# Kernel optimization log

Hardware: AMD Instinct MI355X
Metric: run time of the kernel (lower is better)

Reference implementation:

```python
import jax, jax.numpy as jnp
import numpy as np

E, H, NH = 512, 2048, 8
HD = E // NH
EPS = 1e-5


def setup_inputs() -> dict:
    key = jax.random.key(0)
    ks = jax.random.split(key, 13)
    s = lambda k, shape, fan_in: jax.random.normal(k, shape, dtype=jnp.float32) * (1.0 / np.sqrt(fan_in))
    return {
        "x": jax.random.normal(ks[0], (1, 4096, E), dtype=jnp.float32),
        "ln_g": jnp.ones((E,), jnp.float32),
        "ln_b": jnp.zeros((E,), jnp.float32),
        "qkv_w": s(ks[1], (3 * E, E), E),
        "qkv_b": jnp.zeros((3 * E,), jnp.float32),
        "proj_w": s(ks[2], (E, E), E),
        "proj_b": jnp.zeros((E,), jnp.float32),
        "fc1_w": s(ks[3], (H, E), E),
        "fc1_b": jnp.zeros((H,), jnp.float32),
        "fc2_w": s(ks[4], (H, H), H),
        "fc2_b": jnp.zeros((H,), jnp.float32),
        "fc3_w": s(ks[5], (E, H), H),
        "fc3_b": jnp.zeros((E,), jnp.float32),
    }


def _layernorm(x, g, b):
    mu = jnp.mean(x, axis=-1, keepdims=True)
    var = jnp.mean(jnp.square(x - mu), axis=-1, keepdims=True)
    return (x - mu) * jax.lax.rsqrt(var + EPS) * g + b


def _attention(h, qkv_w, qkv_b, proj_w, proj_b):
    B, N, _ = h.shape
    qkv = h @ qkv_w.T + qkv_b                      # [B, N, 3E]
    qkv = qkv.reshape(B, N, 3, NH, HD).transpose(2, 0, 3, 1, 4)  # [3, B, NH, N, HD]
    q, k, v = qkv[0], qkv[1], qkv[2]
    scale = HD ** -0.5
    scores = jnp.einsum("bhqd,bhkd->bhqk", q, k) * scale  # full N x N matrix (faithful)
    probs = jax.nn.softmax(scores, axis=-1)
    out = jnp.einsum("bhqk,bhkd->bhqd", probs, v)  # [B, NH, N, HD]
    out = out.transpose(0, 2, 1, 3).reshape(B, N, E)
    return out @ proj_w.T + proj_b


def _mlp(h, fc1_w, fc1_b, fc2_w, fc2_b, fc3_w, fc3_b):
    h = jax.nn.relu(h @ fc1_w.T + fc1_b)
    h = jax.nn.relu(h @ fc2_w.T + fc2_b)
    return h @ fc3_w.T + fc3_b


def reference(x, ln_g, ln_b, qkv_w, qkv_b, proj_w, proj_b,
              fc1_w, fc1_b, fc2_w, fc2_b, fc3_w, fc3_b):
    # Pre-norm block; note the SAME LayerNorm params are used for both sublayers
    x = x + _attention(_layernorm(x, ln_g, ln_b), qkv_w, qkv_b, proj_w, proj_b)
    x = x + _mlp(_layernorm(x, ln_g, ln_b), fc1_w, fc1_b, fc2_w, fc2_b, fc3_w, fc3_b)
    return x
```

## Files before the change

kernel.cpp:

```cpp
#include <hip/hip_runtime.h>
#include <cstdint>
#include <cstddef>

typedef _Float16 f16;
typedef f16 f16x8 __attribute__((ext_vector_type(8)));
typedef f16 f16x4 __attribute__((ext_vector_type(4)));
typedef __fp16 h16x2 __attribute__((ext_vector_type(2)));
typedef float f32x4 __attribute__((ext_vector_type(4)));

#define SLEN 4096
#define EDIM 512
#define TEDIM 1536
#define HDIM 2048
#define NHEAD 8
#define HD 64
#define NSPLIT 4

#if __has_builtin(__builtin_amdgcn_exp2f)
#define EXP2(x) __builtin_amdgcn_exp2f(x)
#else
#define EXP2(x) exp2f(x)
#endif

#define LDS_ASYNC16(gp, lp)                                                      \
  __builtin_amdgcn_global_load_lds(                                              \
      (__attribute__((address_space(1))) void*)(void*)(gp),                      \
      (__attribute__((address_space(3))) void*)(void*)(lp), 16, 0, 0)


struct CvtArgs {
  const float* src[5];
  f16* dst[5];
};
__global__ __launch_bounds__(256) void prep_kernel(CvtArgs a, const float* __restrict__ x,
                                                   const float* __restrict__ g,
                                                   const float* __restrict__ bb_,
                                                   f16* __restrict__ h1) {
  int b = blockIdx.x;
  if (b < 3584) {
    int seg, off;
    if (b < 384)       { seg = 0; off = b; }
    else if (b < 512)  { seg = 1; off = b - 384; }
    else if (b < 1024) { seg = 2; off = b - 512; }
    else if (b < 3072) { seg = 3; off = b - 1024; }
    else               { seg = 4; off = b - 3072; }
    int i = (off * 256 + threadIdx.x) * 8;
    const float* src = a.src[seg];
    f16* dst = a.dst[seg];
    float4 p = *(const float4*)(src + i);
    float4 q = *(const float4*)(src + i + 4);
    f16x8 o;
    o[0] = (f16)p.x; o[1] = (f16)p.y; o[2] = (f16)p.z; o[3] = (f16)p.w;
    o[4] = (f16)q.x; o[5] = (f16)q.y; o[6] = (f16)q.z; o[7] = (f16)q.w;
    *(f16x8*)(dst + i) = o;
    return;
  }
  int wave = threadIdx.x >> 6, lane = threadIdx.x & 63;
  int row = (b - 3584) * 4 + wave;
  const float* p = x + (size_t)row * EDIM + lane * 8;
  float v[8];
  float4 aa = *(const float4*)p;
  float4 cc = *(const float4*)(p + 4);
  v[0] = aa.x; v[1] = aa.y; v[2] = aa.z; v[3] = aa.w;
  v[4] = cc.x; v[5] = cc.y; v[6] = cc.z; v[7] = cc.w;
  float s = 0.f, s2 = 0.f;
#pragma unroll
  for (int j = 0; j < 8; ++j) { s += v[j]; s2 += v[j] * v[j]; }
#pragma unroll
  for (int m = 1; m < 64; m <<= 1) {
    s += __shfl_xor(s, m, 64);
    s2 += __shfl_xor(s2, m, 64);
  }
  float mu = s * (1.0f / 512.0f);
  float var = s2 * (1.0f / 512.0f) - mu * mu;
  float rs = rsqrtf(var + 1e-5f);
  float4 gg = *(const float4*)(g + lane * 8);
  float4 gh = *(const float4*)(g + lane * 8 + 4);
  float4 bl = *(const float4*)(bb_ + lane * 8);
  float4 bh = *(const float4*)(bb_ + lane * 8 + 4);
  float ga[8] = {gg.x, gg.y, gg.z, gg.w, gh.x, gh.y, gh.z, gh.w};
  float ba[8] = {bl.x, bl.y, bl.z, bl.w, bh.x, bh.y, bh.z, bh.w};
  f16x8 o;
#pragma unroll
  for (int j = 0; j < 8; ++j) o[j] = (f16)((v[j] - mu) * rs * ga[j] + ba[j]);
  *(f16x8*)(h1 + (size_t)row * EDIM + lane * 8) = o;
}

__global__ __launch_bounds__(256) void ln_kernel(const float* __restrict__ src,
                                                 const float* __restrict__ g,
                                                 const float* __restrict__ b,
                                                 f16* __restrict__ out) {
  int wave = threadIdx.x >> 6, lane = threadIdx.x & 63;
  int row = blockIdx.x * 4 + wave;
  const float* p = src + (size_t)row * EDIM + lane * 8;
  float v[8];
  float4 a = *(const float4*)p;
  float4 c = *(const float4*)(p + 4);
  v[0] = a.x; v[1] = a.y; v[2] = a.z; v[3] = a.w;
  v[4] = c.x; v[5] = c.y; v[6] = c.z; v[7] = c.w;
  float s = 0.f, s2 = 0.f;
#pragma unroll
  for (int j = 0; j < 8; ++j) { s += v[j]; s2 += v[j] * v[j]; }
#pragma unroll
  for (int m = 1; m < 64; m <<= 1) {
    s += __shfl_xor(s, m, 64);
    s2 += __shfl_xor(s2, m, 64);
  }
  float mu = s * (1.0f / 512.0f);
  float var = s2 * (1.0f / 512.0f) - mu * mu;
  float rs = rsqrtf(var + 1e-5f);
  float4 gg = *(const float4*)(g + lane * 8);
  float4 gh = *(const float4*)(g + lane * 8 + 4);
  float4 bb = *(const float4*)(b + lane * 8);
  float4 bh = *(const float4*)(b + lane * 8 + 4);
  float ga[8] = {gg.x, gg.y, gg.z, gg.w, gh.x, gh.y, gh.z, gh.w};
  float ba[8] = {bb.x, bb.y, bb.z, bb.w, bh.x, bh.y, bh.z, bh.w};
  f16x8 o;
#pragma unroll
  for (int j = 0; j < 8; ++j) o[j] = (f16)((v[j] - mu) * rs * ga[j] + ba[j]);
  *(f16x8*)(out + (size_t)row * EDIM + lane * 8) = o;
}

template <int RELU, int RES, int OUTF32, int BM, int BN, int BK>
__global__ __launch_bounds__(256) void gemm_bt(const f16* __restrict__ A,
                                               const f16* __restrict__ W,
                                               const float* __restrict__ bias,
                                               const float* __restrict__ res,
                                               void* __restrict__ out,
                                               int M, int Nn, int K) {
  constexpr int WC = (BM == 128 && BN == 64) ? 1 : 2;
  constexpr int WR = 4 / WC;
  constexpr int MF = BM / (WR * 16);
  constexpr int NF = BN / (WC * 16);
  constexpr int GPR = BK / 8;
  constexpr int RPA = 256 / GPR;
  constexpr int NA_A = BM / RPA;
  constexpr int NA_B = BN / RPA;
  __shared__ f16 lA[BM * BK];
  __shared__ f16 lB[BN * BK];
  const int t = threadIdx.x;
  const int wave = t >> 6, lane = t & 63;
  const int wm = (WC == 1) ? wave : (wave >> 1);
  const int wn = (WC == 1) ? 0 : (wave & 1);
  const int quad = lane >> 4, l15 = lane & 15;
  const int m0 = blockIdx.y * BM, n0 = blockIdx.x * BN;

  f32x4 acc[MF][NF] = {};

  const int srow = t / GPR;
  const int scol = ((t % GPR) ^ (srow & 7)) * 8;
  const f16* gA = A + (size_t)(m0 + srow) * K + scol;
  const f16* gB = W + (size_t)(n0 + srow) * K + scol;
  const int sw = (l15 & 7);

  for (int k0 = 0; k0 < K; k0 += BK) {
    __syncthreads();
#pragma unroll
    for (int is = 0; is < NA_A; ++is)
      LDS_ASYNC16(gA + (size_t)(is * RPA) * K + k0, lA + is * 2048 + wave * 512);
#pragma unroll
    for (int is = 0; is < NA_B; ++is)
      LDS_ASYNC16(gB + (size_t)(is * RPA) * K + k0, lB + is * 2048 + wave * 512);
    __syncthreads();
#pragma unroll
    for (int ks = 0; ks < BK / 32; ++ks) {
      f16x8 af[MF], bfv[NF];
#pragma unroll
      for (int mf = 0; mf < MF; ++mf)
        af[mf] = *(const f16x8*)(lA + (wm * (MF * 16) + mf * 16 + l15) * BK +
                                 ((ks * 4 + quad) ^ sw) * 8);
#pragma unroll
      for (int nf = 0; nf < NF; ++nf)
        bfv[nf] = *(const f16x8*)(lB + (wn * (NF * 16) + nf * 16 + l15) * BK +
                                  ((ks * 4 + quad) ^ sw) * 8);
#pragma unroll
      for (int mf = 0; mf < MF; ++mf)
#pragma unroll
        for (int nf = 0; nf < NF; ++nf)
          acc[mf][nf] =
              __builtin_amdgcn_mfma_f32_16x16x32_f16(af[mf], bfv[nf], acc[mf][nf], 0, 0, 0);
    }
  }

  const int mbase = m0 + wm * (MF * 16);
  const int nbase = n0 + wn * (NF * 16);
  float bv[NF];
#pragma unroll
  for (int nf = 0; nf < NF; ++nf) bv[nf] = bias[nbase + nf * 16 + l15];
#pragma unroll
  for (int mf = 0; mf < MF; ++mf) {
#pragma unroll
    for (int r = 0; r < 4; ++r) {
      size_t m = mbase + mf * 16 + quad * 4 + r;
#pragma unroll
      for (int nf = 0; nf < NF; ++nf) {
        int n = nbase + nf * 16 + l15;
        float v = acc[mf][nf][r] + bv[nf];
        if (RELU) v = v > 0.f ? v : 0.f;
        if (RES) v += res[m * Nn + n];
        if (OUTF32)
          ((float*)out)[m * Nn + n] = v;
        else
          ((f16*)out)[m * Nn + n] = (f16)v;
      }
    }
  }
}

__global__ __launch_bounds__(256) void build_vt(const f16* __restrict__ qkv,
                                                f16* __restrict__ vt) {
  __shared__ f16 tile[64 * 72];
  const int h = blockIdx.x >> 6, nt = blockIdx.x & 63;
  const int t = threadIdx.x;
  const int n0 = nt * 64;
#pragma unroll
  for (int is = 0; is < 2; ++is) {
    int e = is * 2048 + t * 8;
    int nl = e >> 6, d = e & 63;
    f16x8 v = *(const f16x8*)(qkv + (size_t)(n0 + nl) * TEDIM + 1024 + h * 64 + d);
    *(f16x8*)(tile + nl * 72 + d) = v;
  }
  __syncthreads();
  const int d = t >> 2, nc = (t & 3) * 16;
  union { f16 e[16]; f16x8 v[2]; } buf;
#pragma unroll
  for (int j = 0; j < 16; ++j) buf.e[j] = tile[(nc + j) * 72 + d];
  f16* dst = vt + (size_t)h * 64 * SLEN + (size_t)d * SLEN + n0 + nc;
  *(f16x8*)dst = buf.v[0];
  *(f16x8*)(dst + 8) = buf.v[1];
}

__global__ __launch_bounds__(256) void attn_kernel(const f16* __restrict__ qkv,
                                                   const f16* __restrict__ vt,
                                                   f16* __restrict__ Opart,
                                                   float* __restrict__ Lpart) {
  __shared__ f16 lK[64 * 64];
  __shared__ f16 lV[64 * 64];
  const int t = threadIdx.x, wave = t >> 6, lane = t & 63;
  const int quad = lane >> 4, l15 = lane & 15;
  const int split = blockIdx.x & 3;
  const int qb = (blockIdx.x >> 2) & 31;
  const int h = blockIdx.x >> 7;
  const int q0 = qb * 128 + wave * 32;
  const int kv0 = split * (SLEN / NSPLIT);
  const int sw = (l15 & 7);

  f16x8 qf[2][2];
#pragma unroll
  for (int mf = 0; mf < 2; ++mf)
#pragma unroll
    for (int ks = 0; ks < 2; ++ks) {
      f16x8 v = *(const f16x8*)(qkv + (size_t)(q0 + mf * 16 + l15) * TEDIM + h * 64 +
                                ks * 32 + quad * 8);
#pragma unroll
      for (int j = 0; j < 8; ++j) v[j] = v[j] * (f16)0.18033688f;
      qf[mf][ks] = v;
    }

  f32x4 o[2][4] = {};
  f32x4 o5[2] = {};
  f16x4 ones;
#pragma unroll
  for (int j = 0; j < 4; ++j) ones[j] = (l15 == 0) ? (f16)1.0f : (f16)0.0f;

  const int srow = t >> 3;
  const int scol = ((t & 7) ^ (srow & 7)) * 8;
  const f16* gK = qkv + (size_t)(kv0 + srow) * TEDIM + 512 + h * 64 + scol;
  const f16* gV = vt + (size_t)h * 64 * SLEN + (size_t)srow * SLEN + kv0 + scol;

  for (int kt = 0; kt < (SLEN / NSPLIT) / 64; ++kt) {
    __syncthreads();
#pragma unroll
    for (int is = 0; is < 2; ++is) {
      LDS_ASYNC16(gK + (size_t)(kt * 64 + is * 32) * TEDIM, lK + is * 2048 + wave * 512);
      LDS_ASYNC16(gV + (size_t)(is * 32) * SLEN + kt * 64, lV + is * 2048 + wave * 512);
    }
    __syncthreads();

    f32x4 st[4][2] = {};
#pragma unroll
    for (int ks = 0; ks < 2; ++ks) {
      f16x8 kfr[4];
#pragma unroll
      for (int cf = 0; cf < 4; ++cf)
        kfr[cf] = *(const f16x8*)(lK + (cf * 16 + l15) * 64 + ((ks * 4 + quad) ^ sw) * 8);
#pragma unroll
      for (int cf = 0; cf < 4; ++cf)
#pragma unroll
        for (int mf = 0; mf < 2; ++mf)
          st[cf][mf] =
              __builtin_amdgcn_mfma_f32_16x16x32_f16(kfr[cf], qf[mf][ks], st[cf][mf], 0, 0, 0);
    }

    f16x4 pf[4][2];
#pragma unroll
    for (int cf = 0; cf < 4; ++cf)
#pragma unroll
      for (int mf = 0; mf < 2; ++mf)
#pragma unroll
        for (int rp = 0; rp < 2; ++rp) {
          float p0 = EXP2(st[cf][mf][2 * rp]);
          float p1 = EXP2(st[cf][mf][2 * rp + 1]);
          h16x2 pk = __builtin_amdgcn_cvt_pkrtz(p0, p1);
          pf[cf][mf][2 * rp] = (f16)pk[0];
          pf[cf][mf][2 * rp + 1] = (f16)pk[1];
        }

#pragma unroll
    for (int cf = 0; cf < 4; ++cf) {
      f16x4 vfr[4];
#pragma unroll
      for (int nf = 0; nf < 4; ++nf)
        vfr[nf] = *(const f16x4*)(lV + (nf * 16 + l15) * 64 +
                                  (((cf * 2 + (quad >> 1)) ^ sw) * 8) + (quad & 1) * 4);
#pragma unroll
      for (int mf = 0; mf < 2; ++mf) {
#pragma unroll
        for (int nf = 0; nf < 4; ++nf)
          o[mf][nf] = __builtin_amdgcn_mfma_f32_16x16x16f16(pf[cf][mf], vfr[nf], o[mf][nf], 0, 0, 0);
        o5[mf] = __builtin_amdgcn_mfma_f32_16x16x16f16(pf[cf][mf], ones, o5[mf], 0, 0, 0);
      }
    }
  }

  if (l15 == 0) {
#pragma unroll
    for (int mf = 0; mf < 2; ++mf)
#pragma unroll
      for (int r = 0; r < 4; ++r)
        Lpart[(size_t)(split * NHEAD + h) * SLEN + q0 + mf * 16 + quad * 4 + r] = o5[mf][r];
  }
#pragma unroll
  for (int mf = 0; mf < 2; ++mf)
#pragma unroll
    for (int r = 0; r < 4; ++r) {
      int row = q0 + mf * 16 + quad * 4 + r;
      f16* dst = Opart + ((size_t)split * SLEN + row) * EDIM + h * 64;
#pragma unroll
      for (int nf = 0; nf < 4; ++nf) dst[nf * 16 + l15] = (f16)o[mf][nf][r];
    }
}

__global__ __launch_bounds__(256) void attn_combine(const f16* __restrict__ Opart,
                                                    const float* __restrict__ Lpart,
                                                    f16* __restrict__ attn) {
  int idx = (blockIdx.x * 256 + threadIdx.x) * 8;
  int row = idx >> 9;
  int col = idx & 511;
  int h = col >> 6;
  float l = 0.f;
#pragma unroll
  for (int s = 0; s < NSPLIT; ++s) l += Lpart[((size_t)s * NHEAD + h) * SLEN + row];
  float inv = 1.0f / l;
  float acc[8] = {};
#pragma unroll
  for (int s = 0; s < NSPLIT; ++s) {
    f16x8 a = *(const f16x8*)(Opart + ((size_t)s * SLEN + row) * EDIM + col);
#pragma unroll
    for (int j = 0; j < 8; ++j) acc[j] += (float)a[j];
  }
  f16x8 o;
#pragma unroll
  for (int j = 0; j < 8; ++j) o[j] = (f16)(acc[j] * inv);
  *(f16x8*)(attn + (size_t)row * EDIM + col) = o;
}

extern "C" void kernel_launch(void* const* d_in, const int* in_sizes, int n_in,
                              void* d_out, int out_size, void* d_ws, size_t ws_size,
                              hipStream_t stream) {
  const float* x      = (const float*)d_in[0];
  const float* ln_g   = (const float*)d_in[1];
  const float* ln_b   = (const float*)d_in[2];
  const float* qkv_w  = (const float*)d_in[3];
  const float* qkv_b  = (const float*)d_in[4];
  const float* proj_w = (const float*)d_in[5];
  const float* proj_b = (const float*)d_in[6];
  const float* fc1_w  = (const float*)d_in[7];
  const float* fc1_b  = (const float*)d_in[8];
  const float* fc2_w  = (const float*)d_in[9];
  const float* fc2_b  = (const float*)d_in[10];
  const float* fc3_w  = (const float*)d_in[11];
  const float* fc3_b  = (const float*)d_in[12];
  float* out = (float*)d_out;

  char* w = (char*)d_ws;
  f16* wq = (f16*)(w);
  f16* wp = (f16*)(w + (2ull << 20));
  f16* w1 = (f16*)(w + (3ull << 20));
  f16* w2 = (f16*)(w + (5ull << 20));
  f16* w3 = (f16*)(w + (13ull << 20));
  f16* ws_qkv   = (f16*)(w + (15ull << 20));
  f16* ws_vt    = (f16*)(w + (27ull << 20));
  f16* ws_opart = (f16*)(w + (31ull << 20));
  float* ws_lp  = (float*)(w + (47ull << 20));
  f16* ws_attn  = (f16*)(w + (48ull << 20));
  f16* ws_h1    = (f16*)(w + (31ull << 20));
  float* ws_x1  = (float*)(w + (31ull << 20));
  f16* ws_h2    = (f16*)(w + (39ull << 20));
  f16* ws_m1    = (f16*)(w + (15ull << 20));
  f16* ws_m2    = (f16*)(w + (39ull << 20));

  CvtArgs ca;
  ca.src[0] = qkv_w; ca.src[1] = proj_w; ca.src[2] = fc1_w; ca.src[3] = fc2_w; ca.src[4] = fc3_w;
  ca.dst[0] = wq;    ca.dst[1] = wp;     ca.dst[2] = w1;    ca.dst[3] = w2;    ca.dst[4] = w3;
  prep_kernel<<<3584 + SLEN / 4, 256, 0, stream>>>(ca, x, ln_g, ln_b, ws_h1);

  gemm_bt<0, 0, 0, 64, 128, 128><<<dim3(TEDIM / 128, SLEN / 64), 256, 0, stream>>>(
      ws_h1, wq, qkv_b, nullptr, ws_qkv, SLEN, TEDIM, EDIM);
  build_vt<<<NHEAD * (SLEN / 64), 256, 0, stream>>>(ws_qkv, ws_vt);
  attn_kernel<<<NHEAD * (SLEN / 128) * NSPLIT, 256, 0, stream>>>(ws_qkv, ws_vt, ws_opart, ws_lp);
  attn_combine<<<(SLEN * EDIM) / 2048, 256, 0, stream>>>(ws_opart, ws_lp, ws_attn);
  gemm_bt<0, 1, 1, 64, 64, 128><<<dim3(EDIM / 64, SLEN / 64), 256, 0, stream>>>(
      ws_attn, wp, proj_b, x, ws_x1, SLEN, EDIM, EDIM);
  ln_kernel<<<SLEN / 4, 256, 0, stream>>>(ws_x1, ln_g, ln_b, ws_h2);
  gemm_bt<1, 0, 0, 128, 128, 128><<<dim3(HDIM / 128, SLEN / 128), 256, 0, stream>>>(
      ws_h2, w1, fc1_b, nullptr, ws_m1, SLEN, HDIM, EDIM);
  gemm_bt<1, 0, 0, 128, 128, 64><<<dim3(HDIM / 128, SLEN / 128), 256, 0, stream>>>(
      ws_m1, w2, fc2_b, nullptr, ws_m2, SLEN, HDIM, HDIM);
  gemm_bt<0, 1, 1, 64, 64, 64><<<dim3(EDIM / 64, SLEN / 64), 256, 0, stream>>>(
      ws_m2, w3, fc3_b, ws_x1, out, SLEN, EDIM, HDIM);
}
```

Before: 277.8 us.

## Double-buffer LDS tiles in GEMM and attention kernels to overlap loads

The GEMM and attention kernels now keep two LDS buffers each. The next K or KV tile's async global-to-LDS load is issued before computing on the current tile, and the loop uses one barrier per iteration instead of two. The GEMM K-tile is fixed at 64, so the template's BK parameter is dropped and the launches that used BK=128 change tile depth. This is meant to hide global load latency behind MFMA work, at the cost of doubled LDS in attention, which may reduce occupancy.

Measured after the change: 275.4 us. No clear change (-0.9%).

```diff
diff --git a/kernel.cpp b/kernel.cpp
--- a/kernel.cpp
+++ b/kernel.cpp
@@ -121,7 +121,7 @@
   *(f16x8*)(out + (size_t)row * EDIM + lane * 8) = o;
 }
 
-template <int RELU, int RES, int OUTF32, int BM, int BN, int BK>
+template <int RELU, int RES, int OUTF32, int BM, int BN>
 __global__ __launch_bounds__(256) void gemm_bt(const f16* __restrict__ A,
                                                const f16* __restrict__ W,
                                                const float* __restrict__ bias,
@@ -132,12 +132,10 @@
   constexpr int WR = 4 / WC;
   constexpr int MF = BM / (WR * 16);
   constexpr int NF = BN / (WC * 16);
-  constexpr int GPR = BK / 8;
-  constexpr int RPA = 256 / GPR;
-  constexpr int NA_A = BM / RPA;
-  constexpr int NA_B = BN / RPA;
-  __shared__ f16 lA[BM * BK];
-  __shared__ f16 lB[BN * BK];
+  constexpr int NA_A = BM / 32;
+  constexpr int NA_B = BN / 32;
+  __shared__ f16 lA[2][BM * 64];
+  __shared__ f16 lB[2][BN * 64];
   const int t = threadIdx.x;
   const int wave = t >> 6, lane = t & 63;
   const int wm = (WC == 1) ? wave : (wave >> 1);
@@ -147,31 +145,40 @@
 
   f32x4 acc[MF][NF] = {};
 
-  const int srow = t / GPR;
-  const int scol = ((t % GPR) ^ (srow & 7)) * 8;
+  const int srow = t >> 3;
+  const int scol = ((t & 7) ^ (srow & 7)) * 8;
   const f16* gA = A + (size_t)(m0 + srow) * K + scol;
   const f16* gB = W + (size_t)(n0 + srow) * K + scol;
   const int sw = (l15 & 7);
 
-  for (int k0 = 0; k0 < K; k0 += BK) {
+#pragma unroll
+  for (int is = 0; is < NA_A; ++is)
+    LDS_ASYNC16(gA + (size_t)(is * 32) * K, lA[0] + is * 2048 + wave * 512);
+#pragma unroll
+  for (int is = 0; is < NA_B; ++is)
+    LDS_ASYNC16(gB + (size_t)(is * 32) * K, lB[0] + is * 2048 + wave * 512);
+
+  for (int k0 = 0; k0 < K; k0 += 64) {
+    const int cur = (k0 >> 6) & 1, nxt = cur ^ 1;
     __syncthreads();
-#pragma unroll
-    for (int is = 0; is < NA_A; ++is)
-      LDS_ASYNC16(gA + (size_t)(is * RPA) * K + k0, lA + is * 2048 + wave * 512);
-#pragma unroll
-    for (int is = 0; is < NA_B; ++is)
-      LDS_ASYNC16(gB + (size_t)(is * RPA) * K + k0, lB + is * 2048 + wave * 512);
-    __syncthreads();
-#pragma unroll
-    for (int ks = 0; ks < BK / 32; ++ks) {
+    if (k0 + 64 < K) {
+#pragma unroll
+      for (int is = 0; is < NA_A; ++is)
+        LDS_ASYNC16(gA + (size_t)(is * 32) * K + k0 + 64, lA[nxt] + is * 2048 + wave * 512);
+#pragma unroll
+      for (int is = 0; is < NA_B; ++is)
+        LDS_ASYNC16(gB + (size_t)(is * 32) * K + k0 + 64, lB[nxt] + is * 2048 + wave * 512);
+    }
+#pragma unroll
+    for (int ks = 0; ks < 2; ++ks) {
       f16x8 af[MF], bfv[NF];
 #pragma unroll
       for (int mf = 0; mf < MF; ++mf)
-        af[mf] = *(const f16x8*)(lA + (wm * (MF * 16) + mf * 16 + l15) * BK +
+        af[mf] = *(const f16x8*)(lA[cur] + (wm * (MF * 16) + mf * 16 + l15) * 64 +
                                  ((ks * 4 + quad) ^ sw) * 8);
 #pragma unroll
       for (int nf = 0; nf < NF; ++nf)
-        bfv[nf] = *(const f16x8*)(lB + (wn * (NF * 16) + nf * 16 + l15) * BK +
+        bfv[nf] = *(const f16x8*)(lB[cur] + (wn * (NF * 16) + nf * 16 + l15) * 64 +
                                   ((ks * 4 + quad) ^ sw) * 8);
 #pragma unroll
       for (int mf = 0; mf < MF; ++mf)
@@ -234,8 +241,8 @@
                                                    const f16* __restrict__ vt,
                                                    f16* __restrict__ Opart,
                                                    float* __restrict__ Lpart) {
-  __shared__ f16 lK[64 * 64];
-  __shared__ f16 lV[64 * 64];
+  __shared__ f16 lK[2][64 * 64];
+  __shared__ f16 lV[2][64 * 64];
   const int t = threadIdx.x, wave = t >> 6, lane = t & 63;
   const int quad = lane >> 4, l15 = lane & 15;
   const int split = blockIdx.x & 3;
@@ -268,14 +275,25 @@
   const f16* gK = qkv + (size_t)(kv0 + srow) * TEDIM + 512 + h * 64 + scol;
   const f16* gV = vt + (size_t)h * 64 * SLEN + (size_t)srow * SLEN + kv0 + scol;
 
-  for (int kt = 0; kt < (SLEN / NSPLIT) / 64; ++kt) {
+#pragma unroll
+  for (int is = 0; is < 2; ++is) {
+    LDS_ASYNC16(gK + (size_t)(is * 32) * TEDIM, lK[0] + is * 2048 + wave * 512);
+    LDS_ASYNC16(gV + (size_t)(is * 32) * SLEN, lV[0] + is * 2048 + wave * 512);
+  }
+
+  constexpr int NKT = (SLEN / NSPLIT) / 64;
+  for (int kt = 0; kt < NKT; ++kt) {
+    const int cur = kt & 1, nxt = cur ^ 1;
     __syncthreads();
-#pragma unroll
-    for (int is = 0; is < 2; ++is) {
-      LDS_ASYNC16(gK + (size_t)(kt * 64 + is * 32) * TEDIM, lK + is * 2048 + wave * 512);
-      LDS_ASYNC16(gV + (size_t)(is * 32) * SLEN + kt * 64, lV + is * 2048 + wave * 512);
-    }
-    __syncthreads();
+    if (kt + 1 < NKT) {
+#pragma unroll
+      for (int is = 0; is < 2; ++is) {
+        LDS_ASYNC16(gK + (size_t)((kt + 1) * 64 + is * 32) * TEDIM,
+                    lK[nxt] + is * 2048 + wave * 512);
+        LDS_ASYNC16(gV + (size_t)(is * 32) * SLEN + (kt + 1) * 64,
+                    lV[nxt] + is * 2048 + wave * 512);
+      }
+    }
 
     f32x4 st[4][2] = {};
 #pragma unroll
@@ -283,7 +301,7 @@
       f16x8 kfr[4];
 #pragma unroll
       for (int cf = 0; cf < 4; ++cf)
-        kfr[cf] = *(const f16x8*)(lK + (cf * 16 + l15) * 64 + ((ks * 4 + quad) ^ sw) * 8);
+        kfr[cf] = *(const f16x8*)(lK[cur] + (cf * 16 + l15) * 64 + ((ks * 4 + quad) ^ sw) * 8);
 #pragma unroll
       for (int cf = 0; cf < 4; ++cf)
 #pragma unroll
@@ -311,7 +329,7 @@
       f16x4 vfr[4];
 #pragma unroll
       for (int nf = 0; nf < 4; ++nf)
-        vfr[nf] = *(const f16x4*)(lV + (nf * 16 + l15) * 64 +
+        vfr[nf] = *(const f16x4*)(lV[cur] + (nf * 16 + l15) * 64 +
                                   (((cf * 2 + (quad >> 1)) ^ sw) * 8) + (quad & 1) * 4);
 #pragma unroll
       for (int mf = 0; mf < 2; ++mf) {
@@ -405,18 +423,18 @@
   ca.dst[0] = wq;    ca.dst[1] = wp;     ca.dst[2] = w1;    ca.dst[3] = w2;    ca.dst[4] = w3;
   prep_kernel<<<3584 + SLEN / 4, 256, 0, stream>>>(ca, x, ln_g, ln_b, ws_h1);
 
-  gemm_bt<0, 0, 0, 64, 128, 128><<<dim3(TEDIM / 128, SLEN / 64), 256, 0, stream>>>(
+  gemm_bt<0, 0, 0, 64, 128><<<dim3(TEDIM / 128, SLEN / 64), 256, 0, stream>>>(
       ws_h1, wq, qkv_b, nullptr, ws_qkv, SLEN, TEDIM, EDIM);
   build_vt<<<NHEAD * (SLEN / 64), 256, 0, stream>>>(ws_qkv, ws_vt);
   attn_kernel<<<NHEAD * (SLEN / 128) * NSPLIT, 256, 0, stream>>>(ws_qkv, ws_vt, ws_opart, ws_lp);
   attn_combine<<<(SLEN * EDIM) / 2048, 256, 0, stream>>>(ws_opart, ws_lp, ws_attn);
-  gemm_bt<0, 1, 1, 64, 64, 128><<<dim3(EDIM / 64, SLEN / 64), 256, 0, stream>>>(
+  gemm_bt<0, 1, 1, 64, 64><<<dim3(EDIM / 64, SLEN / 64), 256, 0, stream>>>(
       ws_attn, wp, proj_b, x, ws_x1, SLEN, EDIM, EDIM);
   ln_kernel<<<SLEN / 4, 256, 0, stream>>>(ws_x1, ln_g, ln_b, ws_h2);
-  gemm_bt<1, 0, 0, 128, 128, 128><<<dim3(HDIM / 128, SLEN / 128), 256, 0, stream>>>(
+  gemm_bt<1, 0, 0, 128, 128><<<dim3(HDIM / 128, SLEN / 128), 256, 0, stream>>>(
       ws_h2, w1, fc1_b, nullptr, ws_m1, SLEN, HDIM, EDIM);
-  gemm_bt<1, 0, 0, 128, 128, 64><<<dim3(HDIM / 128, SLEN / 128), 256, 0, stream>>>(
+  gemm_bt<1, 0, 0, 128, 128><<<dim3(HDIM / 128, SLEN / 128), 256, 0, stream>>>(
       ws_m1, w2, fc2_b, nullptr, ws_m2, SLEN, HDIM, HDIM);
-  gemm_bt<0, 1, 1, 64, 64, 64><<<dim3(EDIM / 64, SLEN / 64), 256, 0, stream>>>(
+  gemm_bt<0, 1, 1, 64, 64><<<dim3(EDIM / 64, SLEN / 64), 256, 0, stream>>>(
       ws_m2, w3, fc3_b, ws_x1, out, SLEN, EDIM, HDIM);
 }
```

## Fuse V-transpose into QKV GEMM and split-combine into attention via atomic counter

Applied to the files above, without the earlier changes.

The QKV GEMM epilogue now writes V columns directly in transposed layout through an LDS tile, which removes the separate build_vt kernel. The attention kernel increments a per-(head, query block) atomic counter after writing its partials, and the last of the four splits performs the normalized combine itself, which removes the attn_combine launch. This saves two kernel launches and some global round-trips. In exchange it adds a memset launch, threadfences, an atomic per block, and serialized combine work on whichever block finishes last.

Result: slower. 485.6 us (+74.8%).

```diff
diff --git a/kernel.cpp b/kernel.cpp
--- a/kernel.cpp
+++ b/kernel.cpp
@@ -121,12 +121,13 @@
   *(f16x8*)(out + (size_t)row * EDIM + lane * 8) = o;
 }
 
-template <int RELU, int RES, int OUTF32, int BM, int BN, int BK>
+template <int RELU, int RES, int OUTF32, int BM, int BN, int BK, int VTOUT>
 __global__ __launch_bounds__(256) void gemm_bt(const f16* __restrict__ A,
                                                const f16* __restrict__ W,
                                                const float* __restrict__ bias,
                                                const float* __restrict__ res,
                                                void* __restrict__ out,
+                                               f16* __restrict__ vtout,
                                                int M, int Nn, int K) {
   constexpr int WC = (BM == 128 && BN == 64) ? 1 : 2;
   constexpr int WR = 4 / WC;
@@ -187,6 +188,39 @@
   float bv[NF];
 #pragma unroll
   for (int nf = 0; nf < NF; ++nf) bv[nf] = bias[nbase + nf * 16 + l15];
+
+  if (VTOUT && n0 >= 1024) {
+    constexpr int PAD = BN + 8;
+    f16* tile = lB;
+    __syncthreads();
+#pragma unroll
+    for (int mf = 0; mf < MF; ++mf)
+#pragma unroll
+      for (int r = 0; r < 4; ++r) {
+        int lm = wm * (MF * 16) + mf * 16 + quad * 4 + r;
+#pragma unroll
+        for (int nf = 0; nf < NF; ++nf) {
+          int ln = wn * (NF * 16) + nf * 16 + l15;
+          tile[lm * PAD + ln] = (f16)(acc[mf][nf][r] + bv[nf]);
+        }
+      }
+    __syncthreads();
+#pragma unroll
+    for (int p = 0; p < 2; ++p) {
+      int c = p * 64 + (t >> 2);
+      int mchunk = (t & 3) * 16;
+      int nn = n0 - 1024 + c;
+      int h = nn >> 6, d = nn & 63;
+      union { f16 e[16]; f16x8 v[2]; } buf;
+#pragma unroll
+      for (int j = 0; j < 16; ++j) buf.e[j] = tile[(mchunk + j) * PAD + c];
+      f16* dst = vtout + ((size_t)h * 64 + d) * SLEN + m0 + mchunk;
+      *(f16x8*)dst = buf.v[0];
+      *(f16x8*)(dst + 8) = buf.v[1];
+    }
+    return;
+  }
+
 #pragma unroll
   for (int mf = 0; mf < MF; ++mf) {
 #pragma unroll
@@ -207,33 +241,12 @@
   }
 }
 
-__global__ __launch_bounds__(256) void build_vt(const f16* __restrict__ qkv,
-                                                f16* __restrict__ vt) {
-  __shared__ f16 tile[64 * 72];
-  const int h = blockIdx.x >> 6, nt = blockIdx.x & 63;
-  const int t = threadIdx.x;
-  const int n0 = nt * 64;
-#pragma unroll
-  for (int is = 0; is < 2; ++is) {
-    int e = is * 2048 + t * 8;
-    int nl = e >> 6, d = e & 63;
-    f16x8 v = *(const f16x8*)(qkv + (size_t)(n0 + nl) * TEDIM + 1024 + h * 64 + d);
-    *(f16x8*)(tile + nl * 72 + d) = v;
-  }
-  __syncthreads();
-  const int d = t >> 2, nc = (t & 3) * 16;
-  union { f16 e[16]; f16x8 v[2]; } buf;
-#pragma unroll
-  for (int j = 0; j < 16; ++j) buf.e[j] = tile[(nc + j) * 72 + d];
-  f16* dst = vt + (size_t)h * 64 * SLEN + (size_t)d * SLEN + n0 + nc;
-  *(f16x8*)dst = buf.v[0];
-  *(f16x8*)(dst + 8) = buf.v[1];
-}
-
 __global__ __launch_bounds__(256) void attn_kernel(const f16* __restrict__ qkv,
                                                    const f16* __restrict__ vt,
                                                    f16* __restrict__ Opart,
-                                                   float* __restrict__ Lpart) {
+                                                   float* __restrict__ Lpart,
+                                                   f16* __restrict__ attn,
+                                                   int* __restrict__ cnt) {
   __shared__ f16 lK[64 * 64];
   __shared__ f16 lV[64 * 64];
   const int t = threadIdx.x, wave = t >> 6, lane = t & 63;
@@ -339,30 +352,38 @@
 #pragma unroll
       for (int nf = 0; nf < 4; ++nf) dst[nf * 16 + l15] = (f16)o[mf][nf][r];
     }
-}
-
-__global__ __launch_bounds__(256) void attn_combine(const f16* __restrict__ Opart,
-                                                    const float* __restrict__ Lpart,
-                                                    f16* __restrict__ attn) {
-  int idx = (blockIdx.x * 256 + threadIdx.x) * 8;
-  int row = idx >> 9;
-  int col = idx & 511;
-  int h = col >> 6;
-  float l = 0.f;
-#pragma unroll
-  for (int s = 0; s < NSPLIT; ++s) l += Lpart[((size_t)s * NHEAD + h) * SLEN + row];
-  float inv = 1.0f / l;
-  float acc[8] = {};
-#pragma unroll
-  for (int s = 0; s < NSPLIT; ++s) {
-    f16x8 a = *(const f16x8*)(Opart + ((size_t)s * SLEN + row) * EDIM + col);
-#pragma unroll
-    for (int j = 0; j < 8; ++j) acc[j] += (float)a[j];
-  }
-  f16x8 o;
-#pragma unroll
-  for (int j = 0; j < 8; ++j) o[j] = (f16)(acc[j] * inv);
-  *(f16x8*)(attn + (size_t)row * EDIM + col) = o;
+
+  __threadfence();
+  __shared__ int lastflag;
+  if (t == 0) {
+    int old = atomicAdd(&cnt[h * 32 + qb], 1);
+    lastflag = (old == 3);
+  }
+  __syncthreads();
+  if (!lastflag) return;
+  __threadfence();
+#pragma unroll
+  for (int it = 0; it < 4; ++it) {
+    int idx = (it * 256 + t) * 8;
+    int r = idx >> 6;
+    int c = idx & 63;
+    int row = qb * 128 + r;
+    float l = 0.f;
+#pragma unroll
+    for (int s = 0; s < NSPLIT; ++s) l += Lpart[((size_t)s * NHEAD + h) * SLEN + row];
+    float inv = 1.0f / l;
+    float acc[8] = {};
+#pragma unroll
+    for (int s = 0; s < NSPLIT; ++s) {
+      f16x8 a = *(const f16x8*)(Opart + ((size_t)s * SLEN + row) * EDIM + h * 64 + c);
+#pragma unroll
+      for (int j = 0; j < 8; ++j) acc[j] += (float)a[j];
+    }
+    f16x8 ov;
+#pragma unroll
+    for (int j = 0; j < 8; ++j) ov[j] = (f16)(acc[j] * inv);
+    *(f16x8*)(attn + (size_t)row * EDIM + h * 64 + c) = ov;
+  }
 }
 
 extern "C" void kernel_launch(void* const* d_in, const int* in_sizes, int n_in,
@@ -393,6 +414,7 @@
   f16* ws_vt    = (f16*)(w + (27ull << 20));
   f16* ws_opart = (f16*)(w + (31ull << 20));
   float* ws_lp  = (float*)(w + (47ull << 20));
+  int* ws_cnt   = (int*)(w + (47ull << 20) + (512ull << 10));
   f16* ws_attn  = (f16*)(w + (48ull << 20));
   f16* ws_h1    = (f16*)(w + (31ull << 20));
   float* ws_x1  = (float*)(w + (31ull << 20));
@@ -400,23 +422,24 @@
   f16* ws_m1    = (f16*)(w + (15ull << 20));
   f16* ws_m2    = (f16*)(w + (39ull << 20));
 
+  hipMemsetAsync(ws_cnt, 0, NHEAD * 32 * sizeof(int), stream);
+
   CvtArgs ca;
   ca.src[0] = qkv_w; ca.src[1] = proj_w; ca.src[2] = fc1_w; ca.src[3] = fc2_w; ca.src[4] = fc3_w;
   ca.dst[0] = wq;    ca.dst[1] = wp;     ca.dst[2] = w1;    ca.dst[3] = w2;    ca.dst[4] = w3;
   prep_kernel<<<3584 + SLEN / 4, 256, 0, stream>>>(ca, x, ln_g, ln_b, ws_h1);
 
-  gemm_bt<0, 0, 0, 64, 128, 128><<<dim3(TEDIM / 128, SLEN / 64), 256, 0, stream>>>(
-      ws_h1, wq, qkv_b, nullptr, ws_qkv, SLEN, TEDIM, EDIM);
-  build_vt<<<NHEAD * (SLEN / 64), 256, 0, stream>>>(ws_qkv, ws_vt);
-  attn_kernel<<<NHEAD * (SLEN / 128) * NSPLIT, 256, 0, stream>>>(ws_qkv, ws_vt, ws_opart, ws_lp);
-  attn_combine<<<(SLEN * EDIM) / 2048, 256, 0, stream>>>(ws_opart, ws_lp, ws_attn);
-  gemm_bt<0, 1, 1, 64, 64, 128><<<dim3(EDIM / 64, SLEN / 64), 256, 0, stream>>>(
-      ws_attn, wp, proj_b, x, ws_x1, SLEN, EDIM, EDIM);
+  gemm_bt<0, 0, 0, 64, 128, 128, 1><<<dim3(TEDIM / 128, SLEN / 64), 256, 0, stream>>>(
+      ws_h1, wq, qkv_b, nullptr, ws_qkv, ws_vt, SLEN, TEDIM, EDIM);
+  attn_kernel<<<NHEAD * (SLEN / 128) * NSPLIT, 256, 0, stream>>>(
+      ws_qkv, ws_vt, ws_opart, ws_lp, ws_attn, ws_cnt);
+  gemm_bt<0, 1, 1, 64, 64, 128, 0><<<dim3(EDIM / 64, SLEN / 64), 256, 0, stream>>>(
+      ws_attn, wp, proj_b, x, ws_x1, nullptr, SLEN, EDIM, EDIM);
   ln_kernel<<<SLEN / 4, 256, 0, stream>>>(ws_x1, ln_g, ln_b, ws_h2);
-  gemm_bt<1, 0, 0, 128, 128, 128><<<dim3(HDIM / 128, SLEN / 128), 256, 0, stream>>>(
-      ws_h2, w1, fc1_b, nullptr, ws_m1, SLEN, HDIM, EDIM);
-  gemm_bt<1, 0, 0, 128, 128, 64><<<dim3(HDIM / 128, SLEN / 128), 256, 0, stream>>>(
-      ws_m1, w2, fc2_b, nullptr, ws_m2, SLEN, HDIM, HDIM);
-  gemm_bt<0, 1, 1, 64, 64, 64><<<dim3(EDIM / 64, SLEN / 64), 256, 0, stream>>>(
-      ws_m2, w3, fc3_b, ws_x1, out, SLEN, EDIM, HDIM);
+  gemm_bt<1, 0, 0, 128, 128, 128, 0><<<dim3(HDIM / 128, SLEN / 128), 256, 0, stream>>>(
+      ws_h2, w1, fc1_b, nullptr, ws_m1, nullptr, SLEN, HDIM, EDIM);
+  gemm_bt<1, 0, 0, 128, 128, 64, 0><<<dim3(HDIM / 128, SLEN / 128), 256, 0, stream>>>(
+      ws_m1, w2, fc2_b, nullptr, ws_m2, nullptr, SLEN, HDIM, HDIM);
+  gemm_bt<0, 1, 1, 64, 64, 64, 0><<<dim3(EDIM / 64, SLEN / 64), 256, 0, stream>>>(
+      ws_m2, w3, fc3_b, ws_x1, out, nullptr, SLEN, EDIM, HDIM);
 }
```
